# Optimization experiments

Hardware: AMD Instinct MI355X
Metric: run time of the kernel (lower is better)

The kernel has to match this reference:

```python
import jax, jax.numpy as jnp
import numpy as np

N = 8192          # total nodes in the batch of graphs
ATOM = 64         # atom_feats
HID = 128         # hidden_feats
HEADS = 8         # num_heads
NUM_GRAPHS = 256  # number of graphs (max value of `batch`)
NEG_SLOPE = 0.2   # LeakyReLU slope in GAT attention


def setup_inputs() -> dict:
    key = jax.random.key(0)
    ks = jax.random.split(key, 16)
    x = jax.random.normal(ks[0], (N, ATOM), dtype=jnp.float32)
    adj = (jax.random.uniform(ks[1], (N, N)) < 0.01).astype(jnp.float32)
    adj = jnp.maximum(adj, jnp.eye(N, dtype=jnp.float32))
    batch = jnp.sort(jax.random.randint(ks[2], (N,), 0, NUM_GRAPHS)).astype(jnp.int32)

    def u(k, shape, fan_in):
        lim = 1.0 / np.sqrt(fan_in)
        return jax.random.uniform(k, shape, jnp.float32, -lim, lim)

    in1 = HID * HEADS
    params = dict(
        W0=u(ks[3], (ATOM, HID), ATOM), a0_src=u(ks[4], (HID,), HID), a0_dst=u(ks[5], (HID,), HID),
        W1=u(ks[6], (in1, HID), in1), a1_src=u(ks[7], (HID,), HID), a1_dst=u(ks[8], (HID,), HID),
        W2=u(ks[9], (in1, HID), in1), a2_src=u(ks[10], (HID,), HID), a2_dst=u(ks[11], (HID,), HID),
        fc_w=u(ks[12], (HID, 1), HID), fc_b=u(ks[13], (1,), HID),
    )
    return dict(x=x, adj=adj, batch=batch, **params)


def _gat_layer(h_in, W, a_src, a_dst, mask):
    # standard dense GAT: Wh, e_ij = leakyrelu(a_src.Wh_i + a_dst.Wh_j), masked softmax, aggregate
    h = h_in @ W                                         # [N, HID]
    e = jax.nn.leaky_relu((h @ a_src)[:, None] + (h @ a_dst)[None, :], NEG_SLOPE)  # [N, N]
    e = jnp.where(mask, e, jnp.float32(-1e9))
    attn = jax.nn.softmax(e, axis=1)                     # [N, N]
    return attn @ h                                      # [N, HID]


def reference(x, adj, batch, W0, a0_src, a0_dst, W1, a1_src, a1_dst, W2, a2_src, a2_dst, fc_w, fc_b):
    # eval mode: dropout is identity. The torch module calls the SAME layer instance per head,
    # so concat of heads == tile, and the final stacked mean == a single layer call.
    mask = adj > 0
    h0 = _gat_layer(x, W0, a0_src, a0_dst, mask)
    x1 = jax.nn.relu(jnp.tile(h0, (1, HEADS)))           # [N, HID*HEADS]
    h1 = _gat_layer(x1, W1, a1_src, a1_dst, mask)
    x2 = jax.nn.relu(jnp.tile(h1, (1, HEADS)))
    h2 = _gat_layer(x2, W2, a2_src, a2_dst, mask)        # mean over identical heads == h2
    # global mean pool over graphs
    sums = jax.ops.segment_sum(h2, batch, num_segments=NUM_GRAPHS)           # [G, HID]
    cnt = jax.ops.segment_sum(jnp.ones((N, 1), h2.dtype), batch, num_segments=NUM_GRAPHS)
    pooled = sums / jnp.maximum(cnt, 1.0)
    out = pooled @ fc_w + fc_b                           # [G, 1]
    return out[:, 0]
```

## Files before the change

kernel.cpp:

```cpp
#include <hip/hip_runtime.h>
#include <cstdint>
#include <cstddef>

#define NN 8192
#define ATOMF 64
#define HID 128
#define HEADS 8
#define NG 256
#define ELLW 192
#define NEGSLOPE 0.2f

__global__ __launch_bounds__(256) void k_build_ell(const float* __restrict__ adj,
                                                   int* __restrict__ ell,
                                                   int* __restrict__ deg) {
    int row = blockIdx.x;
    int t = threadIdx.x;
    const float4* a4 = (const float4*)(adj + (size_t)row * NN);
    float4 v[8];
    int c = 0;
    #pragma unroll
    for (int it = 0; it < 8; ++it) {
        v[it] = a4[it * 256 + t];
        c += (v[it].x > 0.f) + (v[it].y > 0.f) + (v[it].z > 0.f) + (v[it].w > 0.f);
    }
    __shared__ int cnt[256];
    cnt[t] = c;
    __syncthreads();
    for (int off = 1; off < 256; off <<= 1) {
        int x = (t >= off) ? cnt[t - off] : 0;
        __syncthreads();
        cnt[t] += x;
        __syncthreads();
    }
    int pos = cnt[t] - c;
    int total = cnt[255];
    int* er = ell + (size_t)row * ELLW;
    #pragma unroll
    for (int it = 0; it < 8; ++it) {
        int j0 = (it * 256 + t) * 4;
        if (v[it].x > 0.f && pos < ELLW) { er[pos] = j0;     ++pos; }
        if (v[it].y > 0.f && pos < ELLW) { er[pos] = j0 + 1; ++pos; }
        if (v[it].z > 0.f && pos < ELLW) { er[pos] = j0 + 2; ++pos; }
        if (v[it].w > 0.f && pos < ELLW) { er[pos] = j0 + 3; ++pos; }
    }
    if (t == 0) deg[row] = total < ELLW ? total : ELLW;
}

__global__ __launch_bounds__(256) void k_wreduce(const float* __restrict__ W1,
                                                 const float* __restrict__ W2,
                                                 float* __restrict__ Wr1,
                                                 float* __restrict__ Wr2) {
    int b = blockIdx.x;
    const float* W = (b < 64) ? W1 : W2;
    float* Wr = (b < 64) ? Wr1 : Wr2;
    int i = (b & 63) * 256 + threadIdx.x;
    int k = i >> 7, c = i & 127;
    float s = 0.f;
    #pragma unroll
    for (int h = 0; h < HEADS; ++h)
        s += W[(size_t)(h * HID + k) * HID + c];
    Wr[i] = s;
}

template<int K, bool RELU>
__global__ __launch_bounds__(256) void k_gemm(const float* __restrict__ X,
                                              const float* __restrict__ W,
                                              float* __restrict__ Y) {
    __shared__ float Xl[32 * K];
    int t = threadIdx.x;
    int row0 = blockIdx.x * 32;
    const float4* Xg = (const float4*)(X + (size_t)row0 * K);
    float4* Xl4 = (float4*)Xl;
    #pragma unroll
    for (int i = t; i < 32 * K / 4; i += 256) {
        float4 v = Xg[i];
        if (RELU) {
            v.x = fmaxf(v.x, 0.f); v.y = fmaxf(v.y, 0.f);
            v.z = fmaxf(v.z, 0.f); v.w = fmaxf(v.w, 0.f);
        }
        Xl4[i] = v;
    }
    __syncthreads();
    int cg = t & 31, rg = t >> 5;
    int c0 = cg * 4;
    float acc[4][4];
    #pragma unroll
    for (int r = 0; r < 4; ++r)
        #pragma unroll
        for (int c = 0; c < 4; ++c) acc[r][c] = 0.f;
    for (int k = 0; k < K; k += 4) {
        float4 w0 = *(const float4*)(W + (size_t)(k + 0) * HID + c0);
        float4 w1 = *(const float4*)(W + (size_t)(k + 1) * HID + c0);
        float4 w2 = *(const float4*)(W + (size_t)(k + 2) * HID + c0);
        float4 w3 = *(const float4*)(W + (size_t)(k + 3) * HID + c0);
        #pragma unroll
        for (int r = 0; r < 4; ++r) {
            float4 xv = *(const float4*)(&Xl[(rg * 4 + r) * K + k]);
            acc[r][0] += xv.x * w0.x + xv.y * w1.x + xv.z * w2.x + xv.w * w3.x;
            acc[r][1] += xv.x * w0.y + xv.y * w1.y + xv.z * w2.y + xv.w * w3.y;
            acc[r][2] += xv.x * w0.z + xv.y * w1.z + xv.z * w2.z + xv.w * w3.z;
            acc[r][3] += xv.x * w0.w + xv.y * w1.w + xv.z * w2.w + xv.w * w3.w;
        }
    }
    #pragma unroll
    for (int r = 0; r < 4; ++r)
        *(float4*)(Y + (size_t)(row0 + rg * 4 + r) * HID + c0) =
            make_float4(acc[r][0], acc[r][1], acc[r][2], acc[r][3]);
}

__global__ __launch_bounds__(256) void k_scores(const float* __restrict__ h,
                                                const float* __restrict__ asrc,
                                                const float* __restrict__ adst,
                                                float* __restrict__ ssrc,
                                                float* __restrict__ sdst) {
    int wid = threadIdx.x >> 6;
    int lane = threadIdx.x & 63;
    int row = blockIdx.x * 4 + wid;
    const float* hr = h + (size_t)row * HID;
    float h0 = hr[lane], h1 = hr[lane + 64];
    float ps = h0 * asrc[lane] + h1 * asrc[lane + 64];
    float pd = h0 * adst[lane] + h1 * adst[lane + 64];
    #pragma unroll
    for (int o = 32; o; o >>= 1) {
        ps += __shfl_xor(ps, o);
        pd += __shfl_xor(pd, o);
    }
    if (lane == 0) { ssrc[row] = ps; sdst[row] = pd; }
}

__global__ __launch_bounds__(256, 6) void k_agg(const float* __restrict__ h,
                                                const float* __restrict__ ssrc,
                                                const float* __restrict__ sdst,
                                                const int* __restrict__ ell,
                                                const int* __restrict__ deg,
                                                float* __restrict__ out) {
    __shared__ float wls[4][ELLW];
    __shared__ int jls[4][ELLW];
    int wid = threadIdx.x >> 6;
    int l = threadIdx.x & 63;
    int row = blockIdx.x * 4 + wid;
    float* wl = wls[wid];
    int* jl = jls[wid];
    int d = deg[row];
    float si = ssrc[row];
    const int* er = ell + (size_t)row * ELLW;
    float m = -1e30f;
    for (int k = l; k < d; k += 64) {
        int j = er[k];
        float e = si + sdst[j];
        e = e > 0.f ? e : NEGSLOPE * e;
        jl[k] = j; wl[k] = e;
        m = fmaxf(m, e);
    }
    #pragma unroll
    for (int o = 32; o; o >>= 1) m = fmaxf(m, __shfl_xor(m, o));
    float s = 0.f;
    for (int k = l; k < d; k += 64) {
        float w = __expf(wl[k] - m);
        wl[k] = w;
        s += w;
    }
    #pragma unroll
    for (int o = 32; o; o >>= 1) s += __shfl_xor(s, o);
    float inv = 1.f / s;
    float a0 = 0.f, a1 = 0.f;
    const float* h2l = h + 2 * l;
    int k = 0;
    for (; k + 8 <= d; k += 8) {
        int j0 = jl[k],     j1 = jl[k + 1], j2 = jl[k + 2], j3 = jl[k + 3];
        int j4 = jl[k + 4], j5 = jl[k + 5], j6 = jl[k + 6], j7 = jl[k + 7];
        float w0 = wl[k],     w1 = wl[k + 1], w2 = wl[k + 2], w3 = wl[k + 3];
        float w4 = wl[k + 4], w5 = wl[k + 5], w6 = wl[k + 6], w7 = wl[k + 7];
        float2 v0 = *(const float2*)(h2l + (size_t)j0 * HID);
        float2 v1 = *(const float2*)(h2l + (size_t)j1 * HID);
        float2 v2 = *(const float2*)(h2l + (size_t)j2 * HID);
        float2 v3 = *(const float2*)(h2l + (size_t)j3 * HID);
        float2 v4 = *(const float2*)(h2l + (size_t)j4 * HID);
        float2 v5 = *(const float2*)(h2l + (size_t)j5 * HID);
        float2 v6 = *(const float2*)(h2l + (size_t)j6 * HID);
        float2 v7 = *(const float2*)(h2l + (size_t)j7 * HID);
        a0 += w0 * v0.x; a1 += w0 * v0.y;
        a0 += w1 * v1.x; a1 += w1 * v1.y;
        a0 += w2 * v2.x; a1 += w2 * v2.y;
        a0 += w3 * v3.x; a1 += w3 * v3.y;
        a0 += w4 * v4.x; a1 += w4 * v4.y;
        a0 += w5 * v5.x; a1 += w5 * v5.y;
        a0 += w6 * v6.x; a1 += w6 * v6.y;
        a0 += w7 * v7.x; a1 += w7 * v7.y;
    }
    for (; k < d; ++k) {
        int j = jl[k];
        float w = wl[k];
        float2 v = *(const float2*)(h2l + (size_t)j * HID);
        a0 += w * v.x; a1 += w * v.y;
    }
    float2 o2; o2.x = a0 * inv; o2.y = a1 * inv;
    *(float2*)(out + (size_t)row * HID + 2 * l) = o2;
}

__global__ __launch_bounds__(256) void k_poolfc(const float* __restrict__ h,
                                                const int* __restrict__ batch,
                                                const float* __restrict__ fcw,
                                                const float* __restrict__ fcb,
                                                float* __restrict__ out) {
    int wid = threadIdx.x >> 6, l = threadIdx.x & 63;
    int g = blockIdx.x * 4 + wid;
    int lo = 0, hi = NN;
    while (lo < hi) { int mid = (lo + hi) >> 1; if (batch[mid] < g) lo = mid + 1; else hi = mid; }
    int e0 = lo;
    hi = NN;
    while (lo < hi) { int mid = (lo + hi) >> 1; if (batch[mid] <= g) lo = mid + 1; else hi = mid; }
    int e1 = lo;
    float sum = 0.f;
    for (int r = e0; r < e1; ++r) {
        const float* hr = h + (size_t)r * HID;
        sum += hr[l] * fcw[l] + hr[l + 64] * fcw[l + 64];
    }
    #pragma unroll
    for (int o = 32; o; o >>= 1) sum += __shfl_xor(sum, o);
    if (l == 0) out[g] = sum / fmaxf((float)(e1 - e0), 1.f) + fcb[0];
}

extern "C" void kernel_launch(void* const* d_in, const int* in_sizes, int n_in,
                              void* d_out, int out_size, void* d_ws, size_t ws_size,
                              hipStream_t stream) {
    const float* x    = (const float*)d_in[0];
    const float* adj  = (const float*)d_in[1];
    const int*   batch= (const int*)  d_in[2];
    const float* W0   = (const float*)d_in[3];
    const float* a0s  = (const float*)d_in[4];
    const float* a0d  = (const float*)d_in[5];
    const float* W1   = (const float*)d_in[6];
    const float* a1s  = (const float*)d_in[7];
    const float* a1d  = (const float*)d_in[8];
    const float* W2   = (const float*)d_in[9];
    const float* a2s  = (const float*)d_in[10];
    const float* a2d  = (const float*)d_in[11];
    const float* fcw  = (const float*)d_in[12];
    const float* fcb  = (const float*)d_in[13];
    float* out = (float*)d_out;

    char* ws = (char*)d_ws;
    size_t off = 0;
    auto alloc = [&](size_t bytes) {
        char* p = ws + off;
        off = (off + bytes + 255) & ~255UL;
        return p;
    };
    int*   ell  = (int*)  alloc((size_t)NN * ELLW * 4);
    int*   deg  = (int*)  alloc((size_t)NN * 4);
    float* hA   = (float*)alloc((size_t)NN * HID * 4);
    float* hB   = (float*)alloc((size_t)NN * HID * 4);
    float* ssrc = (float*)alloc((size_t)NN * 4);
    float* sdst = (float*)alloc((size_t)NN * 4);
    float* Wr1  = (float*)alloc((size_t)HID * HID * 4);
    float* Wr2  = (float*)alloc((size_t)HID * HID * 4);
    (void)ws_size; (void)in_sizes; (void)n_in; (void)out_size;

    k_build_ell<<<NN, 256, 0, stream>>>(adj, ell, deg);
    k_wreduce<<<128, 256, 0, stream>>>(W1, W2, Wr1, Wr2);

    k_gemm<ATOMF, false><<<NN / 32, 256, 0, stream>>>(x, W0, hA);
    k_scores<<<NN / 4, 256, 0, stream>>>(hA, a0s, a0d, ssrc, sdst);
    k_agg<<<NN / 4, 256, 0, stream>>>(hA, ssrc, sdst, ell, deg, hB);
    k_gemm<HID, true><<<NN / 32, 256, 0, stream>>>(hB, Wr1, hA);
    k_scores<<<NN / 4, 256, 0, stream>>>(hA, a1s, a1d, ssrc, sdst);
    k_agg<<<NN / 4, 256, 0, stream>>>(hA, ssrc, sdst, ell, deg, hB);
    k_gemm<HID, true><<<NN / 32, 256, 0, stream>>>(hB, Wr2, hA);
    k_scores<<<NN / 4, 256, 0, stream>>>(hA, a2s, a2d, ssrc, sdst);
    k_agg<<<NN / 4, 256, 0, stream>>>(hA, ssrc, sdst, ell, deg, hB);

    k_poolfc<<<NG / 4, 256, 0, stream>>>(hB, batch, fcw, fcb, out);
}
```

Baseline: 210.7 us.

## Fuse ELL build, weight reduce and first GEMM; fuse aggregation with next-layer GEMM

The ELL construction, head-summed weight reduction and first-layer GEMM plus score computation now run in one launch, with blocks dispatched by index range. Each aggregation kernel also performs the next layer's ReLU, row-vector GEMM against the reduced weights and attention-score dot products per wavefront, writing scores into double-buffered arrays. This cuts the launch count from 12 to 5 and removes intermediate round trips of h and the separate score passes. In exchange, the per-row GEMM reads the full 128x128 weight matrix from cache for every row and loses the shared-memory tile reuse of the old blocked GEMM.

```diff
diff --git a/kernel.cpp b/kernel.cpp
--- a/kernel.cpp
+++ b/kernel.cpp
@@ -10,144 +10,126 @@
 #define ELLW 192
 #define NEGSLOPE 0.2f
 
-__global__ __launch_bounds__(256) void k_build_ell(const float* __restrict__ adj,
-                                                   int* __restrict__ ell,
-                                                   int* __restrict__ deg) {
-    int row = blockIdx.x;
-    int t = threadIdx.x;
-    const float4* a4 = (const float4*)(adj + (size_t)row * NN);
-    float4 v[8];
-    int c = 0;
-    #pragma unroll
-    for (int it = 0; it < 8; ++it) {
-        v[it] = a4[it * 256 + t];
-        c += (v[it].x > 0.f) + (v[it].y > 0.f) + (v[it].z > 0.f) + (v[it].w > 0.f);
-    }
-    __shared__ int cnt[256];
-    cnt[t] = c;
-    __syncthreads();
-    for (int off = 1; off < 256; off <<= 1) {
-        int x = (t >= off) ? cnt[t - off] : 0;
+__global__ __launch_bounds__(256, 4) void k_front(
+    const float* __restrict__ adj, const float* __restrict__ x,
+    const float* __restrict__ W0, const float* __restrict__ a0s, const float* __restrict__ a0d,
+    const float* __restrict__ W1, const float* __restrict__ W2,
+    int* __restrict__ ell, int* __restrict__ deg,
+    float* __restrict__ Wr1, float* __restrict__ Wr2,
+    float* __restrict__ g0, float* __restrict__ ssrc, float* __restrict__ sdst) {
+    __shared__ float smem[2048];
+    int b = blockIdx.x, t = threadIdx.x;
+    if (b < NN) {
+        int* cnt = (int*)smem;
+        const float4* a4 = (const float4*)(adj + (size_t)b * NN);
+        float4 v[8];
+        int c = 0;
+        #pragma unroll
+        for (int it = 0; it < 8; ++it) {
+            v[it] = a4[it * 256 + t];
+            c += (v[it].x > 0.f) + (v[it].y > 0.f) + (v[it].z > 0.f) + (v[it].w > 0.f);
+        }
+        cnt[t] = c;
         __syncthreads();
-        cnt[t] += x;
+        for (int off = 1; off < 256; off <<= 1) {
+            int xv = (t >= off) ? cnt[t - off] : 0;
+            __syncthreads();
+            cnt[t] += xv;
+            __syncthreads();
+        }
+        int pos = cnt[t] - c;
+        int total = cnt[255];
+        int* er = ell + (size_t)b * ELLW;
+        #pragma unroll
+        for (int it = 0; it < 8; ++it) {
+            int j0 = (it * 256 + t) * 4;
+            if (v[it].x > 0.f && pos < ELLW) { er[pos] = j0;     ++pos; }
+            if (v[it].y > 0.f && pos < ELLW) { er[pos] = j0 + 1; ++pos; }
+            if (v[it].z > 0.f && pos < ELLW) { er[pos] = j0 + 2; ++pos; }
+            if (v[it].w > 0.f && pos < ELLW) { er[pos] = j0 + 3; ++pos; }
+        }
+        if (t == 0) deg[b] = total < ELLW ? total : ELLW;
+    } else if (b < NN + 128) {
+        int bb = b - NN;
+        const float* W = (bb < 64) ? W1 : W2;
+        float* Wr = (bb < 64) ? Wr1 : Wr2;
+        int i = (bb & 63) * 256 + t;
+        int k = i >> 7, cc = i & 127;
+        float s = 0.f;
+        #pragma unroll
+        for (int h = 0; h < HEADS; ++h) s += W[(size_t)(h * HID + k) * HID + cc];
+        Wr[i] = s;
+    } else {
+        float* Xl = smem;
+        int row0 = (b - NN - 128) * 32;
+        const float4* Xg = (const float4*)(x + (size_t)row0 * ATOMF);
+        float4* Xl4 = (float4*)Xl;
+        #pragma unroll
+        for (int i = t; i < 32 * ATOMF / 4; i += 256) Xl4[i] = Xg[i];
         __syncthreads();
-    }
-    int pos = cnt[t] - c;
-    int total = cnt[255];
-    int* er = ell + (size_t)row * ELLW;
-    #pragma unroll
-    for (int it = 0; it < 8; ++it) {
-        int j0 = (it * 256 + t) * 4;
-        if (v[it].x > 0.f && pos < ELLW) { er[pos] = j0;     ++pos; }
-        if (v[it].y > 0.f && pos < ELLW) { er[pos] = j0 + 1; ++pos; }
-        if (v[it].z > 0.f && pos < ELLW) { er[pos] = j0 + 2; ++pos; }
-        if (v[it].w > 0.f && pos < ELLW) { er[pos] = j0 + 3; ++pos; }
-    }
-    if (t == 0) deg[row] = total < ELLW ? total : ELLW;
-}
-
-__global__ __launch_bounds__(256) void k_wreduce(const float* __restrict__ W1,
-                                                 const float* __restrict__ W2,
-                                                 float* __restrict__ Wr1,
-                                                 float* __restrict__ Wr2) {
-    int b = blockIdx.x;
-    const float* W = (b < 64) ? W1 : W2;
-    float* Wr = (b < 64) ? Wr1 : Wr2;
-    int i = (b & 63) * 256 + threadIdx.x;
-    int k = i >> 7, c = i & 127;
-    float s = 0.f;
-    #pragma unroll
-    for (int h = 0; h < HEADS; ++h)
-        s += W[(size_t)(h * HID + k) * HID + c];
-    Wr[i] = s;
-}
-
-template<int K, bool RELU>
-__global__ __launch_bounds__(256) void k_gemm(const float* __restrict__ X,
-                                              const float* __restrict__ W,
-                                              float* __restrict__ Y) {
-    __shared__ float Xl[32 * K];
-    int t = threadIdx.x;
-    int row0 = blockIdx.x * 32;
-    const float4* Xg = (const float4*)(X + (size_t)row0 * K);
-    float4* Xl4 = (float4*)Xl;
-    #pragma unroll
-    for (int i = t; i < 32 * K / 4; i += 256) {
-        float4 v = Xg[i];
-        if (RELU) {
-            v.x = fmaxf(v.x, 0.f); v.y = fmaxf(v.y, 0.f);
-            v.z = fmaxf(v.z, 0.f); v.w = fmaxf(v.w, 0.f);
-        }
-        Xl4[i] = v;
-    }
-    __syncthreads();
-    int cg = t & 31, rg = t >> 5;
-    int c0 = cg * 4;
-    float acc[4][4];
-    #pragma unroll
-    for (int r = 0; r < 4; ++r)
-        #pragma unroll
-        for (int c = 0; c < 4; ++c) acc[r][c] = 0.f;
-    for (int k = 0; k < K; k += 4) {
-        float4 w0 = *(const float4*)(W + (size_t)(k + 0) * HID + c0);
-        float4 w1 = *(const float4*)(W + (size_t)(k + 1) * HID + c0);
-        float4 w2 = *(const float4*)(W + (size_t)(k + 2) * HID + c0);
-        float4 w3 = *(const float4*)(W + (size_t)(k + 3) * HID + c0);
+        int cg = t & 31, rg = t >> 5;
+        int c0 = cg * 4;
+        float acc[4][4];
+        #pragma unroll
+        for (int r = 0; r < 4; ++r)
+            #pragma unroll
+            for (int c = 0; c < 4; ++c) acc[r][c] = 0.f;
+        for (int k = 0; k < ATOMF; k += 4) {
+            float4 w0 = *(const float4*)(W0 + (size_t)(k + 0) * HID + c0);
+            float4 w1 = *(const float4*)(W0 + (size_t)(k + 1) * HID + c0);
+            float4 w2 = *(const float4*)(W0 + (size_t)(k + 2) * HID + c0);
+            float4 w3 = *(const float4*)(W0 + (size_t)(k + 3) * HID + c0);
+            #pragma unroll
+            for (int r = 0; r < 4; ++r) {
+                float4 xv = *(const float4*)(&Xl[(rg * 4 + r) * ATOMF + k]);
+                acc[r][0] += xv.x * w0.x + xv.y * w1.x + xv.z * w2.x + xv.w * w3.x;
+                acc[r][1] += xv.x * w0.y + xv.y * w1.y + xv.z * w2.y + xv.w * w3.y;
+                acc[r][2] += xv.x * w0.z + xv.y * w1.z + xv.z * w2.z + xv.w * w3.z;
+                acc[r][3] += xv.x * w0.w + xv.y * w1.w + xv.z * w2.w + xv.w * w3.w;
+            }
+        }
+        float4 asv = *(const float4*)(a0s + c0);
+        float4 adv = *(const float4*)(a0d + c0);
         #pragma unroll
         for (int r = 0; r < 4; ++r) {
-            float4 xv = *(const float4*)(&Xl[(rg * 4 + r) * K + k]);
-            acc[r][0] += xv.x * w0.x + xv.y * w1.x + xv.z * w2.x + xv.w * w3.x;
-            acc[r][1] += xv.x * w0.y + xv.y * w1.y + xv.z * w2.y + xv.w * w3.y;
-            acc[r][2] += xv.x * w0.z + xv.y * w1.z + xv.z * w2.z + xv.w * w3.z;
-            acc[r][3] += xv.x * w0.w + xv.y * w1.w + xv.z * w2.w + xv.w * w3.w;
-        }
-    }
-    #pragma unroll
-    for (int r = 0; r < 4; ++r)
-        *(float4*)(Y + (size_t)(row0 + rg * 4 + r) * HID + c0) =
-            make_float4(acc[r][0], acc[r][1], acc[r][2], acc[r][3]);
-}
-
-__global__ __launch_bounds__(256) void k_scores(const float* __restrict__ h,
-                                                const float* __restrict__ asrc,
-                                                const float* __restrict__ adst,
-                                                float* __restrict__ ssrc,
-                                                float* __restrict__ sdst) {
-    int wid = threadIdx.x >> 6;
-    int lane = threadIdx.x & 63;
-    int row = blockIdx.x * 4 + wid;
-    const float* hr = h + (size_t)row * HID;
-    float h0 = hr[lane], h1 = hr[lane + 64];
-    float ps = h0 * asrc[lane] + h1 * asrc[lane + 64];
-    float pd = h0 * adst[lane] + h1 * adst[lane + 64];
-    #pragma unroll
-    for (int o = 32; o; o >>= 1) {
-        ps += __shfl_xor(ps, o);
-        pd += __shfl_xor(pd, o);
-    }
-    if (lane == 0) { ssrc[row] = ps; sdst[row] = pd; }
-}
-
-__global__ __launch_bounds__(256, 6) void k_agg(const float* __restrict__ h,
-                                                const float* __restrict__ ssrc,
-                                                const float* __restrict__ sdst,
-                                                const int* __restrict__ ell,
-                                                const int* __restrict__ deg,
-                                                float* __restrict__ out) {
+            int row = row0 + rg * 4 + r;
+            *(float4*)(g0 + (size_t)row * HID + c0) =
+                make_float4(acc[r][0], acc[r][1], acc[r][2], acc[r][3]);
+            float ps = acc[r][0] * asv.x + acc[r][1] * asv.y + acc[r][2] * asv.z + acc[r][3] * asv.w;
+            float pd = acc[r][0] * adv.x + acc[r][1] * adv.y + acc[r][2] * adv.z + acc[r][3] * adv.w;
+            #pragma unroll
+            for (int o = 16; o; o >>= 1) {
+                ps += __shfl_xor(ps, o);
+                pd += __shfl_xor(pd, o);
+            }
+            if (cg == 0) { ssrc[row] = ps; sdst[row] = pd; }
+        }
+    }
+}
+
+template<int DO_GEMM>
+__global__ __launch_bounds__(256, 4) void k_layer(
+    const float* __restrict__ g, const float* __restrict__ ssrc_in,
+    const float* __restrict__ sdst_in,
+    const int* __restrict__ ell, const int* __restrict__ deg,
+    const float* __restrict__ Wr, const float* __restrict__ as_,
+    const float* __restrict__ ad_,
+    float* __restrict__ gout, float* __restrict__ ssrc_out,
+    float* __restrict__ sdst_out) {
     __shared__ float wls[4][ELLW];
     __shared__ int jls[4][ELLW];
-    int wid = threadIdx.x >> 6;
-    int l = threadIdx.x & 63;
+    __shared__ float xls[4][HID];
+    int wid = threadIdx.x >> 6, l = threadIdx.x & 63;
     int row = blockIdx.x * 4 + wid;
     float* wl = wls[wid];
     int* jl = jls[wid];
     int d = deg[row];
-    float si = ssrc[row];
+    float si = ssrc_in[row];
     const int* er = ell + (size_t)row * ELLW;
     float m = -1e30f;
     for (int k = l; k < d; k += 64) {
         int j = er[k];
-        float e = si + sdst[j];
+        float e = si + sdst_in[j];
         e = e > 0.f ? e : NEGSLOPE * e;
         jl[k] = j; wl[k] = e;
         m = fmaxf(m, e);
@@ -164,7 +146,7 @@
     for (int o = 32; o; o >>= 1) s += __shfl_xor(s, o);
     float inv = 1.f / s;
     float a0 = 0.f, a1 = 0.f;
-    const float* h2l = h + 2 * l;
+    const float* h2l = g + 2 * l;
     int k = 0;
     for (; k + 8 <= d; k += 8) {
         int j0 = jl[k],     j1 = jl[k + 1], j2 = jl[k + 2], j3 = jl[k + 3];
@@ -194,8 +176,38 @@
         float2 v = *(const float2*)(h2l + (size_t)j * HID);
         a0 += w * v.x; a1 += w * v.y;
     }
-    float2 o2; o2.x = a0 * inv; o2.y = a1 * inv;
-    *(float2*)(out + (size_t)row * HID + 2 * l) = o2;
+    a0 *= inv; a1 *= inv;
+    if (DO_GEMM == 0) {
+        *(float2*)(gout + (size_t)row * HID + 2 * l) = make_float2(a0, a1);
+        return;
+    }
+    float* xl = xls[wid];
+    xl[2 * l]     = fmaxf(a0, 0.f);
+    xl[2 * l + 1] = fmaxf(a1, 0.f);
+    float acc0 = 0.f, acc1 = 0.f;
+    for (int kk = 0; kk < HID; kk += 4) {
+        float4 xv = *(const float4*)(&xl[kk]);
+        float wa0 = Wr[(size_t)(kk + 0) * HID + l];
+        float wb0 = Wr[(size_t)(kk + 0) * HID + l + 64];
+        float wa1 = Wr[(size_t)(kk + 1) * HID + l];
+        float wb1 = Wr[(size_t)(kk + 1) * HID + l + 64];
+        float wa2 = Wr[(size_t)(kk + 2) * HID + l];
+        float wb2 = Wr[(size_t)(kk + 2) * HID + l + 64];
+        float wa3 = Wr[(size_t)(kk + 3) * HID + l];
+        float wb3 = Wr[(size_t)(kk + 3) * HID + l + 64];
+        acc0 += xv.x * wa0 + xv.y * wa1 + xv.z * wa2 + xv.w * wa3;
+        acc1 += xv.x * wb0 + xv.y * wb1 + xv.z * wb2 + xv.w * wb3;
+    }
+    gout[(size_t)row * HID + l]      = acc0;
+    gout[(size_t)row * HID + l + 64] = acc1;
+    float ps = acc0 * as_[l] + acc1 * as_[l + 64];
+    float pd = acc0 * ad_[l] + acc1 * ad_[l + 64];
+    #pragma unroll
+    for (int o = 32; o; o >>= 1) {
+        ps += __shfl_xor(ps, o);
+        pd += __shfl_xor(pd, o);
+    }
+    if (l == 0) { ssrc_out[row] = ps; sdst_out[row] = pd; }
 }
 
 __global__ __launch_bounds__(256) void k_poolfc(const float* __restrict__ h,
@@ -251,24 +263,21 @@
     int*   deg  = (int*)  alloc((size_t)NN * 4);
     float* hA   = (float*)alloc((size_t)NN * HID * 4);
     float* hB   = (float*)alloc((size_t)NN * HID * 4);
-    float* ssrc = (float*)alloc((size_t)NN * 4);
-    float* sdst = (float*)alloc((size_t)NN * 4);
+    float* sAs  = (float*)alloc((size_t)NN * 4);
+    float* sAd  = (float*)alloc((size_t)NN * 4);
+    float* sBs  = (float*)alloc((size_t)NN * 4);
+    float* sBd  = (float*)alloc((size_t)NN * 4);
     float* Wr1  = (float*)alloc((size_t)HID * HID * 4);
     float* Wr2  = (float*)alloc((size_t)HID * HID * 4);
     (void)ws_size; (void)in_sizes; (void)n_in; (void)out_size;
 
-    k_build_ell<<<NN, 256, 0, stream>>>(adj, ell, deg);
-    k_wreduce<<<128, 256, 0, stream>>>(W1, W2, Wr1, Wr2);
-
-    k_gemm<ATOMF, false><<<NN / 32, 256, 0, stream>>>(x, W0, hA);
-    k_scores<<<NN / 4, 256, 0, stream>>>(hA, a0s, a0d, ssrc, sdst);
-    k_agg<<<NN / 4, 256, 0, stream>>>(hA, ssrc, sdst, ell, deg, hB);
-    k_gemm<HID, true><<<NN / 32, 256, 0, stream>>>(hB, Wr1, hA);
-    k_scores<<<NN / 4, 256, 0, stream>>>(hA, a1s, a1d, ssrc, sdst);
-    k_agg<<<NN / 4, 256, 0, stream>>>(hA, ssrc, sdst, ell, deg, hB);
-    k_gemm<HID, true><<<NN / 32, 256, 0, stream>>>(hB, Wr2, hA);
-    k_scores<<<NN / 4, 256, 0, stream>>>(hA, a2s, a2d, ssrc, sdst);
-    k_agg<<<NN / 4, 256, 0, stream>>>(hA, ssrc, sdst, ell, deg, hB);
-
+    k_front<<<NN + 128 + 256, 256, 0, stream>>>(adj, x, W0, a0s, a0d, W1, W2,
+                                                ell, deg, Wr1, Wr2, hA, sAs, sAd);
+    k_layer<1><<<NN / 4, 256, 0, stream>>>(hA, sAs, sAd, ell, deg, Wr1, a1s, a1d,
+                                           hB, sBs, sBd);
+    k_layer<1><<<NN / 4, 256, 0, stream>>>(hB, sBs, sBd, ell, deg, Wr2, a2s, a2d,
+                                           hA, sAs, sAd);
+    k_layer<0><<<NN / 4, 256, 0, stream>>>(hA, sAs, sAd, ell, deg, nullptr, nullptr,
+                                           nullptr, hB, nullptr, nullptr);
     k_poolfc<<<NG / 4, 256, 0, stream>>>(hB, batch, fcw, fcb, out);
 }
```

New measurement: 319.0 us. 1.51x slower.
